# Kernel optimization log

Hardware: AMD Instinct MI355X
Metric: run time of the kernel (lower is better)

## Reference

```python
import jax, jax.numpy as jnp
import numpy as np

MODEL_DIM = 1024
NUM_HEADS = 16
K_DIM = MODEL_DIM // NUM_HEADS


def setup_inputs() -> dict:
    key = jax.random.key(0)
    k1, k2, k3 = jax.random.split(key, 3)
    x = jax.random.normal(k1, (4, 2048, MODEL_DIM), dtype=jnp.float32)
    # nn.Linear(model_dim, 3*model_dim, bias=False): store as [D, 3D] so y = x @ W
    wqkv = jax.random.normal(k2, (MODEL_DIM, 3 * MODEL_DIM), dtype=jnp.float32) * (MODEL_DIM ** -0.5)
    wo = jax.random.normal(k3, (MODEL_DIM, MODEL_DIM), dtype=jnp.float32) * (MODEL_DIM ** -0.5)
    return {"x": x, "wqkv": wqkv, "wo": wo}


def reference(x, wqkv, wo):
    B, L, D = x.shape
    H, K = NUM_HEADS, K_DIM
    qkv = jnp.einsum("bld,de->ble", x, wqkv)  # [B, L, 3D]
    q, k, v = jnp.split(qkv, 3, axis=-1)
    # Faithful to source: plain reshape (no transpose) into [B, H, L, K]
    qh = q.reshape(B, H, L, K)
    kh = k.reshape(B, H, L, K)
    vh = v.reshape(B, H, L, K)
    scores = jnp.einsum("bhlk,bhmk->bhlm", qh, kh) / jnp.sqrt(jnp.float32(K))
    # Faithful quirk: softmax over dim=1 (head axis), as in the source
    probs = jax.nn.softmax(scores, axis=1)
    attended = jnp.einsum("bhlm,bhmk->bhlk", probs, vh)  # [B, H, L, K]
    concatted = attended.transpose(0, 2, 1, 3).reshape(B, L, D)
    return jnp.einsum("bld,de->ble", concatted, wo)
```

## Files before the change

### kernel.cpp

```cpp
#include <hip/hip_runtime.h>
#include <hip/hip_bf16.h>
#include <stdint.h>

typedef __attribute__((ext_vector_type(8))) short short8;
typedef __attribute__((ext_vector_type(4))) float floatx4;

#define QSCALE 0.18033688f

__device__ __forceinline__ unsigned short f2bf(float f) {
    unsigned int u = __float_as_uint(f);
    u += 0x7fffu + ((u >> 16) & 1u);
    return (unsigned short)(u >> 16);
}
__device__ __forceinline__ unsigned int pack2bf(float a, float b) {
    __hip_bfloat162 h = __float22bfloat162_rn(make_float2(a, b));
    return *reinterpret_cast<unsigned int*>(&h);
}

__device__ __forceinline__ void async16(const void* g, void* l) {
    __builtin_amdgcn_global_load_lds(
        (const __attribute__((address_space(1))) unsigned int*)g,
        (__attribute__((address_space(3))) unsigned int*)l, 16, 0, 0);
}

__global__ __launch_bounds__(256) void cvt_bf16(const float* __restrict__ src,
                                                unsigned short* __restrict__ dst, int n8) {
    int i = blockIdx.x * 256 + threadIdx.x;
    if (i >= n8) return;
    const float4 a = ((const float4*)src)[2 * i];
    const float4 b = ((const float4*)src)[2 * i + 1];
    ushort4 lo, hi;
    lo.x = f2bf(a.x); lo.y = f2bf(a.y); lo.z = f2bf(a.z); lo.w = f2bf(a.w);
    hi.x = f2bf(b.x); hi.y = f2bf(b.y); hi.z = f2bf(b.z); hi.w = f2bf(b.w);
    ((ushort4*)dst)[2 * i] = lo;
    ((ushort4*)dst)[2 * i + 1] = hi;
}

__global__ __launch_bounds__(256) void tcvt(const float* __restrict__ src,
                                            unsigned short* __restrict__ dst, int R, int C) {
    __shared__ unsigned short t[64][72];
    const int tid = threadIdx.x;
    const int r0 = blockIdx.y * 64, c0 = blockIdx.x * 64;
    #pragma unroll
    for (int it = 0; it < 4; it++) {
        int idx = it * 256 + tid;
        int rr = idx >> 4, cc = (idx & 15) * 4;
        float4 v = *(const float4*)(src + (size_t)(r0 + rr) * C + c0 + cc);
        t[cc + 0][rr] = f2bf(v.x);
        t[cc + 1][rr] = f2bf(v.y);
        t[cc + 2][rr] = f2bf(v.z);
        t[cc + 3][rr] = f2bf(v.w);
    }
    __syncthreads();
    #pragma unroll
    for (int it = 0; it < 2; it++) {
        int idx = it * 256 + tid;
        int cc = idx >> 3, r8 = (idx & 7) * 8;
        short8 v = *(const short8*)&t[cc][r8];
        *(short8*)(dst + (size_t)(c0 + cc) * R + r0 + r8) = v;
    }
}

__global__ __launch_bounds__(256) void vtrans(const unsigned short* __restrict__ vb,
                                              unsigned short* __restrict__ vbt) {
    __shared__ unsigned short t[64][72];
    const int tid = threadIdx.x;
    const int bh = blockIdx.y, m0 = blockIdx.x * 64;
    const unsigned short* src = vb + ((size_t)bh * 2048 + m0) * 64;
    unsigned short* dst = vbt + ((size_t)bh << 17) + m0;
    union { short8 v; unsigned short u[8]; } tmp;
    #pragma unroll
    for (int it = 0; it < 2; it++) {
        int idx = it * 256 + tid;
        int m = idx >> 3, c8 = (idx & 7) * 8;
        tmp.v = *(const short8*)(src + (size_t)m * 64 + c8);
        #pragma unroll
        for (int j = 0; j < 8; j++) t[c8 + j][m] = tmp.u[j];
    }
    __syncthreads();
    #pragma unroll
    for (int it = 0; it < 2; it++) {
        int idx = it * 256 + tid;
        int k = idx >> 3, c8 = (idx & 7) * 8;
        short8 v = *(const short8*)&t[k][c8];
        *(short8*)(dst + (size_t)k * 2048 + c8) = v;
    }
}

__global__ __launch_bounds__(256) void qkv_gemm(
    const unsigned short* __restrict__ A, const unsigned short* __restrict__ Bt,
    unsigned short* __restrict__ qb, unsigned short* __restrict__ kb,
    unsigned short* __restrict__ vb)
{
    __shared__ __align__(16) unsigned short As[128 * 32];
    __shared__ __align__(16) unsigned short Bs[128 * 32];
    const int tid = threadIdx.x, wave = tid >> 6, lane = tid & 63;
    const int quad = lane >> 4, lr = lane & 15;
    const int wr = wave >> 1, wc = wave & 1;
    const int bm = blockIdx.y * 128, bn = blockIdx.x * 128;
    const int lrow = lane >> 2, lcol = (lane & 3) * 8;

    floatx4 acc[4][4];
    #pragma unroll
    for (int i = 0; i < 4; i++)
        #pragma unroll
        for (int j = 0; j < 4; j++) acc[i][j] = (floatx4)0.0f;

    for (int k0 = 0; k0 < 1024; k0 += 32) {
        #pragma unroll
        for (int t = 0; t < 2; t++) {
            const int rbase = wave * 32 + t * 16;
            const int r = rbase + lrow;
            async16(A  + (size_t)(bm + r) * 1024 + k0 + lcol, &As[rbase * 32]);
            async16(Bt + (size_t)(bn + r) * 1024 + k0 + lcol, &Bs[rbase * 32]);
        }
        __syncthreads();
        short8 af[4], bfr[4];
        #pragma unroll
        for (int i = 0; i < 4; i++)
            af[i] = *(const short8*)&As[(wr * 64 + i * 16 + lr) * 32 + quad * 8];
        #pragma unroll
        for (int j = 0; j < 4; j++)
            bfr[j] = *(const short8*)&Bs[(wc * 64 + j * 16 + lr) * 32 + quad * 8];
        #pragma unroll
        for (int i = 0; i < 4; i++)
            #pragma unroll
            for (int j = 0; j < 4; j++)
                acc[i][j] = __builtin_amdgcn_mfma_f32_16x16x32_bf16(af[i], bfr[j], acc[i][j], 0, 0, 0);
        __syncthreads();
    }

    const int part = bn >> 10;
    unsigned short* __restrict__ dstb = (part == 0) ? qb : ((part == 1) ? kb : vb);
    const float sc = (part == 0) ? QSCALE : 1.0f;
    const int dbase = bn & 1023;
    #pragma unroll
    for (int i = 0; i < 4; i++)
        #pragma unroll
        for (int j = 0; j < 4; j++)
            #pragma unroll
            for (int r = 0; r < 4; r++) {
                int row = bm + wr * 64 + i * 16 + quad * 4 + r;
                int d   = dbase + wc * 64 + j * 16 + lr;
                int b = row >> 11, l = row & 2047;
                int flat = (l << 10) | d;
                int h = flat >> 17;
                int rem = flat & 131071;
                int l2 = rem >> 6, kk = rem & 63;
                dstb[((size_t)(b * 16 + h) * 2048 + l2) * 64 + kk] = f2bf(acc[i][j][r] * sc);
            }
}

__global__ __launch_bounds__(256) void out_gemm(
    const unsigned short* __restrict__ A, const unsigned short* __restrict__ Bt,
    float* __restrict__ C)
{
    __shared__ __align__(16) unsigned short As[128 * 32];
    __shared__ __align__(16) unsigned short Bs[128 * 32];
    const int tid = threadIdx.x, wave = tid >> 6, lane = tid & 63;
    const int quad = lane >> 4, lr = lane & 15;
    const int wr = wave >> 1, wc = wave & 1;
    const int bm = blockIdx.y * 128, bn = blockIdx.x * 128;
    const int lrow = lane >> 2, lcol = (lane & 3) * 8;

    floatx4 acc[4][4];
    #pragma unroll
    for (int i = 0; i < 4; i++)
        #pragma unroll
        for (int j = 0; j < 4; j++) acc[i][j] = (floatx4)0.0f;

    for (int k0 = 0; k0 < 1024; k0 += 32) {
        #pragma unroll
        for (int t = 0; t < 2; t++) {
            const int rbase = wave * 32 + t * 16;
            const int r = rbase + lrow;
            async16(A  + (size_t)(bm + r) * 1024 + k0 + lcol, &As[rbase * 32]);
            async16(Bt + (size_t)(bn + r) * 1024 + k0 + lcol, &Bs[rbase * 32]);
        }
        __syncthreads();
        short8 af[4], bfr[4];
        #pragma unroll
        for (int i = 0; i < 4; i++)
            af[i] = *(const short8*)&As[(wr * 64 + i * 16 + lr) * 32 + quad * 8];
        #pragma unroll
        for (int j = 0; j < 4; j++)
            bfr[j] = *(const short8*)&Bs[(wc * 64 + j * 16 + lr) * 32 + quad * 8];
        #pragma unroll
        for (int i = 0; i < 4; i++)
            #pragma unroll
            for (int j = 0; j < 4; j++)
                acc[i][j] = __builtin_amdgcn_mfma_f32_16x16x32_bf16(af[i], bfr[j], acc[i][j], 0, 0, 0);
        __syncthreads();
    }
    #pragma unroll
    for (int i = 0; i < 4; i++)
        #pragma unroll
        for (int j = 0; j < 4; j++)
            #pragma unroll
            for (int r = 0; r < 4; r++) {
                int row = bm + wr * 64 + i * 16 + quad * 4 + r;
                int col = bn + wc * 64 + j * 16 + lr;
                C[(size_t)row * 1024 + col] = acc[i][j][r];
            }
}

__global__ __launch_bounds__(256, 5) void attn_denom(
    const unsigned short* __restrict__ qb, const unsigned short* __restrict__ kb,
    unsigned short* __restrict__ drpT)
{
    __shared__ __align__(16) unsigned short Qs[2][64 * 64];
    __shared__ __align__(16) unsigned short Ks[2][64 * 64];
    const int tid = threadIdx.x, wave = tid >> 6, lane = tid & 63;
    const int quad = lane >> 4, lr = lane & 15;
    const int e7 = lr & 7;
    const int M0 = blockIdx.x * 64, L0 = blockIdx.y * 64, b = blockIdx.z;

    const int klr = lane >> 3;
    const int ksw8 = ((lane & 7) ^ klr) * 8;
    const size_t hb0 = ((size_t)(b * 16)) << 17;
    const unsigned short* qsrc0 = qb + hb0 + (size_t)(L0 + wave * 8 + klr) * 64 + ksw8;
    const unsigned short* ksrc0 = kb + hb0 + (size_t)(M0 + wave * 8 + klr) * 64 + ksw8;

    floatx4 e[4];
    #pragma unroll
    for (int i = 0; i < 4; i++) e[i] = (floatx4)0.0f;

    async16(qsrc0,           &Qs[0][(wave * 8) * 64]);
    async16(qsrc0 + 32 * 64, &Qs[0][(32 + wave * 8) * 64]);
    async16(ksrc0,           &Ks[0][(wave * 8) * 64]);
    async16(ksrc0 + 32 * 64, &Ks[0][(32 + wave * 8) * 64]);
    __syncthreads();

    for (int h = 0; h < 16; h++) {
        const int cur = h & 1, nxt = cur ^ 1;
        if (h < 15) {
            const unsigned short* qs = qsrc0 + ((size_t)(h + 1) << 17);
            const unsigned short* ks = ksrc0 + ((size_t)(h + 1) << 17);
            async16(qs,           &Qs[nxt][(wave * 8) * 64]);
            async16(qs + 32 * 64, &Qs[nxt][(32 + wave * 8) * 64]);
            async16(ks,           &Ks[nxt][(wave * 8) * 64]);
            async16(ks + 32 * 64, &Ks[nxt][(32 + wave * 8) * 64]);
        }
        const unsigned short* qsp = &Qs[cur][0];
        const unsigned short* ksp = &Ks[cur][0];
        const int rq = wave * 16 + lr;
        short8 qf0 = *(const short8*)&qsp[rq * 64 + (quad ^ e7) * 8];
        short8 qf1 = *(const short8*)&qsp[rq * 64 + ((4 + quad) ^ e7) * 8];
        #pragma unroll
        for (int mt = 0; mt < 4; mt++) {
            const int rk = mt * 16 + lr;
            short8 kf0 = *(const short8*)&ksp[rk * 64 + (quad ^ e7) * 8];
            short8 kf1 = *(const short8*)&ksp[rk * 64 + ((4 + quad) ^ e7) * 8];
            floatx4 s = (floatx4)0.0f;
            __builtin_amdgcn_s_setprio(1);
            s = __builtin_amdgcn_mfma_f32_16x16x32_bf16(kf0, qf0, s, 0, 0, 0);
            s = __builtin_amdgcn_mfma_f32_16x16x32_bf16(kf1, qf1, s, 0, 0, 0);
            __builtin_amdgcn_s_setprio(0);
            e[mt][0] += __builtin_amdgcn_exp2f(s[0]);
            e[mt][1] += __builtin_amdgcn_exp2f(s[1]);
            e[mt][2] += __builtin_amdgcn_exp2f(s[2]);
            e[mt][3] += __builtin_amdgcn_exp2f(s[3]);
        }
        if (h < 15) __syncthreads();
    }
    #pragma unroll
    for (int mt = 0; mt < 4; mt++) {
        float r0 = __builtin_amdgcn_rcpf(e[mt][0]);
        float r1 = __builtin_amdgcn_rcpf(e[mt][1]);
        float r2 = __builtin_amdgcn_rcpf(e[mt][2]);
        float r3 = __builtin_amdgcn_rcpf(e[mt][3]);
        uint2 o;
        o.x = pack2bf(r0, r1);
        o.y = pack2bf(r2, r3);
        int mtg = (M0 >> 4) + mt;
        int ltg = (L0 >> 4) + wave;
        *(uint2*)(drpT + ((((size_t)b * 128 + mtg) * 128 + ltg) << 8) + lane * 4) = o;
    }
}

__global__ __launch_bounds__(256, 3) void attn_pv(
    const unsigned short* __restrict__ qb, const unsigned short* __restrict__ kb,
    const unsigned short* __restrict__ vbt, const unsigned short* __restrict__ drpT,
    unsigned short* __restrict__ cb)
{
    __shared__ __align__(16) unsigned short Ks[2][64 * 64];
    __shared__ __align__(16) unsigned short Vs[2][64 * 64];
    __shared__ __align__(16) unsigned short Ps[128 * 64];
    const int tid = threadIdx.x, wave = tid >> 6, lane = tid & 63;
    const int quad = lane >> 4, lr = lane & 15;
    const int e7 = lr & 7;
    const int flat = blockIdx.x;
    const int swz = (flat & 7) * 128 + (flat >> 3);
    const int Lt = swz & 15;
    const int h = (swz >> 4) & 15;
    const int b = swz >> 8;
    const int L0 = Lt * 128;
    const size_t head = (size_t)(b * 16 + h);
    const unsigned short* qbase = qb + (head << 17);
    const unsigned short* kbase = kb + (head << 17);
    const unsigned short* vtb   = vbt + (head << 17);
    const unsigned short* dbase = drpT + (((size_t)b * 128 * 128 + (L0 >> 4) + wave * 2) << 8) + lane * 4;

    const int klr = lane >> 3;
    const int ksw = (lane & 7) ^ klr;
    const unsigned short* ksrc0 = kbase + (size_t)(wave * 8 + klr) * 64 + ksw * 8;
    const unsigned short* vsrc0 = vtb + (size_t)(wave * 8 + klr) * 2048 + ksw * 8;

    short8 qf[2][2];
    #pragma unroll
    for (int j = 0; j < 2; j++) {
        const unsigned short* qr = qbase + (size_t)(L0 + wave * 32 + j * 16 + lr) * 64;
        qf[j][0] = *(const short8*)(qr + quad * 8);
        qf[j][1] = *(const short8*)(qr + 32 + quad * 8);
    }

    floatx4 oacc[2][4];
    #pragma unroll
    for (int i = 0; i < 2; i++)
        #pragma unroll
        for (int j = 0; j < 4; j++) oacc[i][j] = (floatx4)0.0f;

    async16(ksrc0,             &Ks[0][(wave * 8) * 64]);
    async16(ksrc0 + 32 * 64,   &Ks[0][(32 + wave * 8) * 64]);
    async16(vsrc0,             &Vs[0][(wave * 8) * 64]);
    async16(vsrc0 + 32 * 2048, &Vs[0][(32 + wave * 8) * 64]);
    uint2 du[4][2];
    #pragma unroll
    for (int mt = 0; mt < 4; mt++)
        #pragma unroll
        for (int j = 0; j < 2; j++)
            du[mt][j] = *(const uint2*)(dbase + ((size_t)mt << 15) + (j << 8));
    __syncthreads();

    for (int t = 0; t < 32; t++) {
        const int M0 = t * 64;
        const int cur = t & 1, nxt = cur ^ 1;
        uint2 dun[4][2];
        if (t < 31) {
            const unsigned short* ks = ksrc0 + (size_t)(M0 + 64) * 64;
            const unsigned short* vs = vsrc0 + (M0 + 64);
            async16(ks,             &Ks[nxt][(wave * 8) * 64]);
            async16(ks + 32 * 64,   &Ks[nxt][(32 + wave * 8) * 64]);
            async16(vs,             &Vs[nxt][(wave * 8) * 64]);
            async16(vs + 32 * 2048, &Vs[nxt][(32 + wave * 8) * 64]);
            #pragma unroll
            for (int mt = 0; mt < 4; mt++)
                #pragma unroll
                for (int j = 0; j < 2; j++)
                    dun[mt][j] = *(const uint2*)(dbase + (((size_t)((t + 1) * 4 + mt)) << 15) + (j << 8));
        }
        __builtin_amdgcn_sched_barrier(0);
        const unsigned short* ksp = &Ks[cur][0];
        #pragma unroll
        for (int mt = 0; mt < 4; mt++) {
            const int rk = mt * 16 + lr;
            short8 kf0 = *(const short8*)&ksp[rk * 64 + (quad ^ e7) * 8];
            short8 kf1 = *(const short8*)&ksp[rk * 64 + ((4 + quad) ^ e7) * 8];
            #pragma unroll
            for (int j = 0; j < 2; j++) {
                uint2 duv = du[mt][j];
                floatx4 s = (floatx4)0.0f;
                __builtin_amdgcn_s_setprio(1);
                s = __builtin_amdgcn_mfma_f32_16x16x32_bf16(kf0, qf[j][0], s, 0, 0, 0);
                s = __builtin_amdgcn_mfma_f32_16x16x32_bf16(kf1, qf[j][1], s, 0, 0, 0);
                __builtin_amdgcn_s_setprio(0);
                float r0 = __uint_as_float(duv.x << 16);
                float r1 = __uint_as_float(duv.x & 0xffff0000u);
                float r2 = __uint_as_float(duv.y << 16);
                float r3 = __uint_as_float(duv.y & 0xffff0000u);
                float p0 = __builtin_amdgcn_exp2f(s[0]) * r0;
                float p1 = __builtin_amdgcn_exp2f(s[1]) * r1;
                float p2 = __builtin_amdgcn_exp2f(s[2]) * r2;
                float p3 = __builtin_amdgcn_exp2f(s[3]) * r3;
                uint2 o;
                o.x = pack2bf(p0, p1);
                o.y = pack2bf(p2, p3);
                const int l_loc = wave * 32 + j * 16 + lr;
                const int lb16 = mt * 2 + (quad >> 1);
                *(uint2*)&Ps[l_loc * 64 + (lb16 ^ e7) * 8 + (quad & 1) * 4] = o;
            }
        }
        const unsigned short* vsp = &Vs[cur][0];
        #pragma unroll
        for (int f = 0; f < 2; f++) {
            short8 pf[2], vf[4];
            #pragma unroll
            for (int i2 = 0; i2 < 2; i2++)
                pf[i2] = *(const short8*)&Ps[(wave * 32 + i2 * 16 + lr) * 64 + ((f * 4 + quad) ^ e7) * 8];
            #pragma unroll
            for (int j2 = 0; j2 < 4; j2++) {
                const int rv = j2 * 16 + lr;
                vf[j2] = *(const short8*)&vsp[rv * 64 + ((f * 4 + quad) ^ e7) * 8];
            }
            __builtin_amdgcn_s_setprio(1);
            #pragma unroll
            for (int j2 = 0; j2 < 4; j2++)
                #pragma unroll
                for (int i2 = 0; i2 < 2; i2++)
                    oacc[i2][j2] = __builtin_amdgcn_mfma_f32_16x16x32_bf16(
                        pf[i2], vf[j2], oacc[i2][j2], 0, 0, 0);
            __builtin_amdgcn_s_setprio(0);
        }
        if (t < 31) {
            #pragma unroll
            for (int mt = 0; mt < 4; mt++)
                #pragma unroll
                for (int j = 0; j < 2; j++)
                    du[mt][j] = dun[mt][j];
            __syncthreads();
        }
    }
    #pragma unroll
    for (int i2 = 0; i2 < 2; i2++)
        #pragma unroll
        for (int j2 = 0; j2 < 4; j2++)
            #pragma unroll
            for (int r = 0; r < 4; r++) {
                int row = L0 + wave * 32 + i2 * 16 + quad * 4 + r;
                int col = h * 64 + j2 * 16 + lr;
                cb[(size_t)(b * 2048 + row) * 1024 + col] = f2bf(oacc[i2][j2][r]);
            }
}

extern "C" void kernel_launch(void* const* d_in, const int* in_sizes, int n_in,
                              void* d_out, int out_size, void* d_ws, size_t ws_size,
                              hipStream_t stream) {
    const float* x    = (const float*)d_in[0];
    const float* wqkv = (const float*)d_in[1];
    const float* wo   = (const float*)d_in[2];
    float* out = (float*)d_out;

    unsigned short* W = (unsigned short*)d_ws;
    unsigned short* qb   = W;
    unsigned short* kb   = W + 8388608;
    unsigned short* vbt  = W + 16777216;
    unsigned short* drpT = W + 25165824;
    unsigned short* cb   = W + 41943040;
    unsigned short* xb    = drpT;
    unsigned short* wqkvT = drpT + 8388608;
    unsigned short* vb    = cb;
    unsigned short* woT   = drpT;

    cvt_bf16  <<<4096, 256, 0, stream>>>(x, xb, 1048576);
    tcvt      <<<dim3(48, 16), 256, 0, stream>>>(wqkv, wqkvT, 1024, 3072);
    qkv_gemm  <<<dim3(24, 64), 256, 0, stream>>>(xb, wqkvT, qb, kb, vb);
    vtrans    <<<dim3(32, 64), 256, 0, stream>>>(vb, vbt);
    attn_denom<<<dim3(32, 32, 4), 256, 0, stream>>>(qb, kb, drpT);
    attn_pv   <<<1024, 256, 0, stream>>>(qb, kb, vbt, drpT, cb);
    tcvt      <<<dim3(16, 16), 256, 0, stream>>>(wo, woT, 1024, 1024);
    out_gemm  <<<dim3(8, 64), 256, 0, stream>>>(cb, woT, out);
}
```

Baseline: 370.4 us.

## Rotate three shared K/V buffers in attn_pv to raise occupancy to four blocks

Replaces the double-buffered K and V tiles (four 8KB buffers) with a rotating set of three 8KB buffers, splitting the prefetch so the next K tile loads at iteration start and the next V tile loads after the score phase into the freed K buffer. The denominator prefetch registers (dun) are removed by loading du directly mid-iteration, and launch bounds go from 3 to 4 blocks per CU. The aim is to cut LDS and register use so more waves hide latency. The cost is an extra __syncthreads per iteration and a shorter window for the V and denominator loads to land before use.

Measured after the change: 353.7 us. 1.05x faster.

```diff
diff --git a/kernel.cpp b/kernel.cpp
--- a/kernel.cpp
+++ b/kernel.cpp
@@ -278,13 +278,12 @@
     }
 }
 
-__global__ __launch_bounds__(256, 3) void attn_pv(
+__global__ __launch_bounds__(256, 4) void attn_pv(
     const unsigned short* __restrict__ qb, const unsigned short* __restrict__ kb,
     const unsigned short* __restrict__ vbt, const unsigned short* __restrict__ drpT,
     unsigned short* __restrict__ cb)
 {
-    __shared__ __align__(16) unsigned short Ks[2][64 * 64];
-    __shared__ __align__(16) unsigned short Vs[2][64 * 64];
+    __shared__ __align__(16) unsigned short KV[3][64 * 64];
     __shared__ __align__(16) unsigned short Ps[128 * 64];
     const int tid = threadIdx.x, wave = tid >> 6, lane = tid & 63;
     const int quad = lane >> 4, lr = lane & 15;
@@ -320,10 +319,10 @@
         #pragma unroll
         for (int j = 0; j < 4; j++) oacc[i][j] = (floatx4)0.0f;
 
-    async16(ksrc0,             &Ks[0][(wave * 8) * 64]);
-    async16(ksrc0 + 32 * 64,   &Ks[0][(32 + wave * 8) * 64]);
-    async16(vsrc0,             &Vs[0][(wave * 8) * 64]);
-    async16(vsrc0 + 32 * 2048, &Vs[0][(32 + wave * 8) * 64]);
+    async16(ksrc0,             &KV[0][(wave * 8) * 64]);
+    async16(ksrc0 + 32 * 64,   &KV[0][(32 + wave * 8) * 64]);
+    async16(vsrc0,             &KV[1][(wave * 8) * 64]);
+    async16(vsrc0 + 32 * 2048, &KV[1][(32 + wave * 8) * 64]);
     uint2 du[4][2];
     #pragma unroll
     for (int mt = 0; mt < 4; mt++)
@@ -332,25 +331,15 @@
             du[mt][j] = *(const uint2*)(dbase + ((size_t)mt << 15) + (j << 8));
     __syncthreads();
 
+    int kcur = 0, vcur = 1, sp = 2;
     for (int t = 0; t < 32; t++) {
         const int M0 = t * 64;
-        const int cur = t & 1, nxt = cur ^ 1;
-        uint2 dun[4][2];
         if (t < 31) {
             const unsigned short* ks = ksrc0 + (size_t)(M0 + 64) * 64;
-            const unsigned short* vs = vsrc0 + (M0 + 64);
-            async16(ks,             &Ks[nxt][(wave * 8) * 64]);
-            async16(ks + 32 * 64,   &Ks[nxt][(32 + wave * 8) * 64]);
-            async16(vs,             &Vs[nxt][(wave * 8) * 64]);
-            async16(vs + 32 * 2048, &Vs[nxt][(32 + wave * 8) * 64]);
-            #pragma unroll
-            for (int mt = 0; mt < 4; mt++)
-                #pragma unroll
-                for (int j = 0; j < 2; j++)
-                    dun[mt][j] = *(const uint2*)(dbase + (((size_t)((t + 1) * 4 + mt)) << 15) + (j << 8));
-        }
-        __builtin_amdgcn_sched_barrier(0);
-        const unsigned short* ksp = &Ks[cur][0];
+            async16(ks,           &KV[sp][(wave * 8) * 64]);
+            async16(ks + 32 * 64, &KV[sp][(32 + wave * 8) * 64]);
+        }
+        const unsigned short* ksp = &KV[kcur][0];
         #pragma unroll
         for (int mt = 0; mt < 4; mt++) {
             const int rk = mt * 16 + lr;
@@ -380,7 +369,19 @@
                 *(uint2*)&Ps[l_loc * 64 + (lb16 ^ e7) * 8 + (quad & 1) * 4] = o;
             }
         }
-        const unsigned short* vsp = &Vs[cur][0];
+        if (t < 31) {
+            __syncthreads();
+            const unsigned short* vs = vsrc0 + (M0 + 64);
+            async16(vs,             &KV[kcur][(wave * 8) * 64]);
+            async16(vs + 32 * 2048, &KV[kcur][(32 + wave * 8) * 64]);
+            #pragma unroll
+            for (int mt = 0; mt < 4; mt++)
+                #pragma unroll
+                for (int j = 0; j < 2; j++)
+                    du[mt][j] = *(const uint2*)(dbase + (((size_t)((t + 1) * 4 + mt)) << 15) + (j << 8));
+        }
+        __builtin_amdgcn_sched_barrier(0);
+        const unsigned short* vsp = &KV[vcur][0];
         #pragma unroll
         for (int f = 0; f < 2; f++) {
             short8 pf[2], vf[4];
@@ -402,12 +403,11 @@
             __builtin_amdgcn_s_setprio(0);
         }
         if (t < 31) {
-            #pragma unroll
-            for (int mt = 0; mt < 4; mt++)
-                #pragma unroll
-                for (int j = 0; j < 2; j++)
-                    du[mt][j] = dun[mt][j];
             __syncthreads();
+            const int ok = kcur;
+            kcur = sp;
+            sp = vcur;
+            vcur = ok;
         }
     }
     #pragma unroll
```
